# Performance work log

Measured on AMD Instinct MI355X. Metric: run time of the kernel, lower is better.

## Reference

```python
import jax, jax.numpy as jnp
import numpy as np

B, H, S, D = 8, 8, 1024, 64

def setup_inputs() -> dict:
    key = jax.random.key(0)
    kq, kk, kv = jax.random.split(key, 3)
    queries = jax.random.normal(kq, (B, H, S, D), dtype=jnp.float32)
    keys = jax.random.normal(kk, (B, H, S, D), dtype=jnp.float32)
    values = jax.random.normal(kv, (B, H, S, D), dtype=jnp.float32)
    return {"queries": queries, "keys": keys, "values": values}

def reference(queries, keys, values):
    # scale = 1/sqrt(D) since self.scale is None
    scale = 1.0 / jnp.sqrt(jnp.asarray(queries.shape[-1], queries.dtype))
    # scores: [B, H, S, S]
    scores = jnp.einsum("bhqd,bhkd->bhqk", queries, keys) * scale
    # mask_flag=False -> no masking; dropout treated as identity (eval mode)
    attn = jax.nn.softmax(scores, axis=-1)
    output = jnp.einsum("bhqk,bhkd->bhqd", attn, values)
    return (output, attn)
```

## Files before the change

kernel.cpp:

```cpp
#include <hip/hip_runtime.h>
#include <hip/hip_bf16.h>

#define B_ 8
#define H_ 8
#define S_ 1024
#define D_ 64

typedef __attribute__((ext_vector_type(8))) short bf16x8;
typedef __attribute__((ext_vector_type(4))) short bf16x4;
typedef __attribute__((ext_vector_type(4))) float f32x4;

__device__ __forceinline__ short f2bf(float f) {
  union { float f; unsigned u; } x; x.f = f;
  unsigned r = (x.u + 0x7FFFu + ((x.u >> 16) & 1u)) >> 16;
  return (short)r;
}

__global__ __launch_bounds__(256) void cvt_qk(const float* __restrict__ Q,
                                              const float* __restrict__ K,
                                              short* __restrict__ Qb,
                                              short* __restrict__ Kb) {
  const float* in = blockIdx.y ? K : Q;
  short* out      = blockIdx.y ? Kb : Qb;
  const size_t i = ((size_t)blockIdx.x * 256 + threadIdx.x) * 8;
  float4 a = *(const float4*)(in + i);
  float4 b = *(const float4*)(in + i + 4);
  bf16x8 f;
  f[0] = f2bf(a.x); f[1] = f2bf(a.y); f[2] = f2bf(a.z); f[3] = f2bf(a.w);
  f[4] = f2bf(b.x); f[5] = f2bf(b.y); f[6] = f2bf(b.z); f[7] = f2bf(b.w);
  *(bf16x8*)(out + i) = f;
}

__global__ __launch_bounds__(256) void vtrans(const float* __restrict__ V,
                                              short* __restrict__ Vt) {
  const int bh = blockIdx.y;
  const int s0 = blockIdx.x * 64;
  __shared__ float tile[64][65];
  const float* Vb = V + ((size_t)bh * S_ + s0) * D_;
  const int t = threadIdx.x;
  {
    const int rbase = t >> 4;
    const int c4 = (t & 15) * 4;
    #pragma unroll
    for (int i = 0; i < 4; ++i) {
      const int row = i * 16 + rbase;
      float4 v = *(const float4*)(Vb + (size_t)row * D_ + c4);
      tile[row][c4 + 0] = v.x; tile[row][c4 + 1] = v.y;
      tile[row][c4 + 2] = v.z; tile[row][c4 + 3] = v.w;
    }
  }
  __syncthreads();
  const int d = t >> 2;
  const int sq = (t & 3) * 16;
  short* op = Vt + ((size_t)bh * D_ + d) * S_ + s0 + sq;
  bf16x8 a, b;
  #pragma unroll
  for (int j = 0; j < 8; ++j) {
    a[j] = f2bf(tile[sq + j][d]);
    b[j] = f2bf(tile[sq + 8 + j][d]);
  }
  *(bf16x8*)op = a;
  *(bf16x8*)(op + 8) = b;
}

constexpr int QT  = 16;
constexpr int NW  = 4;
constexpr int TPW = (S_ / 16) / NW;

__global__ __launch_bounds__(256, 4) void attn_fused(
    const short* __restrict__ Qb16, const short* __restrict__ Kb16,
    const short* __restrict__ Vt,
    float* __restrict__ O, float* __restrict__ A)
{
  const int nwg = (S_ / QT) * B_ * H_;
  const int cpx = nwg / 8;
  const int lin = blockIdx.x;
  const int swz = (lin & 7) * cpx + (lin >> 3);
  const int bh  = swz / (S_ / QT);
  const int q0  = (swz % (S_ / QT)) * QT;

  const int tid  = threadIdx.x;
  const int wave = tid >> 6;
  const int lane = tid & 63;
  const int m    = lane & 15;
  const int quad = lane >> 4;

  const short* Qb  = Qb16 + (size_t)bh * S_ * D_;
  const short* Kb  = Kb16 + (size_t)bh * S_ * D_;
  const short* Vtb = Vt   + (size_t)bh * D_ * S_;
  float* Ob = O + (size_t)bh * S_ * D_;
  float* Ab = A + (size_t)bh * S_ * S_;

  __shared__ float redmax[NW][QT];
  __shared__ float redsum[NW][QT];
  __shared__ float obuf[NW][QT][D_ + 4];

  bf16x8 qf0, qf1;
  {
    const short* qp = Qb + (size_t)(q0 + m) * D_ + quad * 8;
    qf0 = *(const bf16x8*)qp;
    qf1 = *(const bf16x8*)(qp + 32);
  }

  const short* kbase = Kb + (size_t)m * D_ + quad * 8;
  f32x4 acc[TPW];
  bf16x8 ka0[4], ka1[4];
  #pragma unroll
  for (int p = 0; p < 3; ++p) {
    const short* kp = kbase + (size_t)((p * NW + wave) * 16) * D_;
    ka0[p] = *(const bf16x8*)kp;
    ka1[p] = *(const bf16x8*)(kp + 32);
  }
  #pragma unroll
  for (int t = 0; t < TPW; ++t) {
    if (t + 3 < TPW) {
      const short* kp = kbase + (size_t)(((t + 3) * NW + wave) * 16) * D_;
      ka0[(t + 3) & 3] = *(const bf16x8*)kp;
      ka1[(t + 3) & 3] = *(const bf16x8*)(kp + 32);
    }
    f32x4 c = {0.f, 0.f, 0.f, 0.f};
    c = __builtin_amdgcn_mfma_f32_16x16x32_bf16(ka0[t & 3], qf0, c, 0, 0, 0);
    c = __builtin_amdgcn_mfma_f32_16x16x32_bf16(ka1[t & 3], qf1, c, 0, 0, 0);
    acc[t] = c;
  }

  float mx[TPW];
  #pragma unroll
  for (int t = 0; t < TPW; ++t)
    mx[t] = fmaxf(fmaxf(acc[t][0], acc[t][1]), fmaxf(acc[t][2], acc[t][3]));
  #pragma unroll
  for (int sstep = TPW / 2; sstep > 0; sstep >>= 1) {
    #pragma unroll
    for (int t = 0; t < sstep; ++t) mx[t] = fmaxf(mx[t], mx[t + sstep]);
  }
  float vmax = mx[0];
  vmax = fmaxf(vmax, __shfl_xor(vmax, 16));
  vmax = fmaxf(vmax, __shfl_xor(vmax, 32));

  constexpr float CE = 0.125f * 1.4426950408889634f;
  float sm[TPW];
  #pragma unroll
  for (int t = 0; t < TPW; ++t) {
    float e0 = __builtin_exp2f((acc[t][0] - vmax) * CE);
    float e1 = __builtin_exp2f((acc[t][1] - vmax) * CE);
    float e2 = __builtin_exp2f((acc[t][2] - vmax) * CE);
    float e3 = __builtin_exp2f((acc[t][3] - vmax) * CE);
    acc[t][0] = e0; acc[t][1] = e1; acc[t][2] = e2; acc[t][3] = e3;
    sm[t] = (e0 + e1) + (e2 + e3);
  }
  #pragma unroll
  for (int sstep = TPW / 2; sstep > 0; sstep >>= 1) {
    #pragma unroll
    for (int t = 0; t < sstep; ++t) sm[t] += sm[t + sstep];
  }
  float psum = sm[0];
  psum += __shfl_xor(psum, 16);
  psum += __shfl_xor(psum, 32);

  if (lane < 16) {
    redmax[wave][lane] = vmax;
    redsum[wave][lane] = psum;
  }
  __syncthreads();

  float m0 = redmax[0][m], m1 = redmax[1][m], m2 = redmax[2][m], m3 = redmax[3][m];
  const float gmax = fmaxf(fmaxf(m0, m1), fmaxf(m2, m3));
  float sumg = redsum[0][m] * __builtin_exp2f((m0 - gmax) * CE)
             + redsum[1][m] * __builtin_exp2f((m1 - gmax) * CE)
             + redsum[2][m] * __builtin_exp2f((m2 - gmax) * CE)
             + redsum[3][m] * __builtin_exp2f((m3 - gmax) * CE);
  const float rinv = __builtin_exp2f((vmax - gmax) * CE) / sumg;

  const short* vbase = Vtb + (size_t)m * S_ + quad * 4;
  bf16x4 vb[4][4];
  #pragma unroll
  for (int p = 0; p < 3; ++p) {
    const short* vp = vbase + (p * NW + wave) * 16;
    #pragma unroll
    for (int i = 0; i < 4; ++i)
      vb[p][i] = *(const bf16x4*)(vp + (size_t)(16 * i) * S_);
  }

  f32x4 oc0 = {0.f,0.f,0.f,0.f}, oc1 = {0.f,0.f,0.f,0.f};
  f32x4 oc2 = {0.f,0.f,0.f,0.f}, oc3 = {0.f,0.f,0.f,0.f};
  float* arow = Ab + (size_t)(q0 + m) * S_ + quad * 4;
  #pragma unroll
  for (int t = 0; t < TPW; ++t) {
    if (t + 3 < TPW) {
      const short* vp = vbase + ((t + 3) * NW + wave) * 16;
      #pragma unroll
      for (int i = 0; i < 4; ++i)
        vb[(t + 3) & 3][i] = *(const bf16x4*)(vp + (size_t)(16 * i) * S_);
    }
    const int kt = t * NW + wave;
    f32x4 pn = acc[t] * rinv;
    __builtin_nontemporal_store(pn, (f32x4*)(arow + kt * 16));
    bf16x4 pa;
    pa[0] = f2bf(pn[0]); pa[1] = f2bf(pn[1]);
    pa[2] = f2bf(pn[2]); pa[3] = f2bf(pn[3]);
    oc0 = __builtin_amdgcn_mfma_f32_16x16x16bf16_1k(pa, vb[t & 3][0], oc0, 0, 0, 0);
    oc1 = __builtin_amdgcn_mfma_f32_16x16x16bf16_1k(pa, vb[t & 3][1], oc1, 0, 0, 0);
    oc2 = __builtin_amdgcn_mfma_f32_16x16x16bf16_1k(pa, vb[t & 3][2], oc2, 0, 0, 0);
    oc3 = __builtin_amdgcn_mfma_f32_16x16x16bf16_1k(pa, vb[t & 3][3], oc3, 0, 0, 0);
  }

  #pragma unroll
  for (int r = 0; r < 4; ++r) {
    obuf[wave][quad * 4 + r][m]      = oc0[r];
    obuf[wave][quad * 4 + r][16 + m] = oc1[r];
    obuf[wave][quad * 4 + r][32 + m] = oc2[r];
    obuf[wave][quad * 4 + r][48 + m] = oc3[r];
  }
  __syncthreads();
  {
    const int q  = tid >> 4;
    const int d4 = (tid & 15) * 4;
    f32x4 o0 = *(const f32x4*)&obuf[0][q][d4];
    f32x4 o1 = *(const f32x4*)&obuf[1][q][d4];
    f32x4 o2 = *(const f32x4*)&obuf[2][q][d4];
    f32x4 o3 = *(const f32x4*)&obuf[3][q][d4];
    f32x4 o = (o0 + o1) + (o2 + o3);
    *(f32x4*)&Ob[(size_t)(q0 + q) * D_ + d4] = o;
  }
}

extern "C" void kernel_launch(void* const* d_in, const int* in_sizes, int n_in,
                              void* d_out, int out_size, void* d_ws, size_t ws_size,
                              hipStream_t stream) {
  const float* Q = (const float*)d_in[0];
  const float* K = (const float*)d_in[1];
  const float* V = (const float*)d_in[2];
  float* O = (float*)d_out;
  float* A = O + (size_t)B_ * H_ * S_ * D_;

  const size_t NEL = (size_t)B_ * H_ * S_ * D_;
  short* Qbf = (short*)d_ws;
  short* Kbf = Qbf + NEL;
  short* Vtb = Kbf + NEL;

  const int cvt_blocks = (int)(NEL / 8 / 256);
  cvt_qk<<<dim3(cvt_blocks, 2), 256, 0, stream>>>(Q, K, Qbf, Kbf);
  vtrans<<<dim3(S_ / 64, B_ * H_), 256, 0, stream>>>(V, Vtb);

  attn_fused<<<(S_ / QT) * B_ * H_, NW * 64, 0, stream>>>(Qbf, Kbf, Vtb, O, A);
}
```

Baseline: 471.5 us.

## Stage attention-probability rows through LDS for coalesced full-row stores

Remaps each wave's key tiles to contiguous 64-column blocks within 256-column groups. Each group of normalized probabilities is staged into a double-buffered LDS chunk, then written to global memory as coalesced 1 KB row segments. The old path issued scattered 16-byte nontemporal stores per lane. The change also drops the register prefetch ring for V fragments and loads them inline, and adds a block barrier per group, which may expose more load latency.

Result: faster. 459.3 us (-2.6%).

```diff
diff --git a/kernel.cpp b/kernel.cpp
--- a/kernel.cpp
+++ b/kernel.cpp
@@ -66,6 +66,7 @@
 constexpr int QT  = 16;
 constexpr int NW  = 4;
 constexpr int TPW = (S_ / 16) / NW;
+constexpr int CH_STRIDE = 260;
 
 __global__ __launch_bounds__(256, 4) void attn_fused(
     const short* __restrict__ Qb16, const short* __restrict__ Kb16,
@@ -91,9 +92,9 @@
   float* Ob = O + (size_t)bh * S_ * D_;
   float* Ab = A + (size_t)bh * S_ * S_;
 
+  __shared__ float smem[2 * 16 * CH_STRIDE];
   __shared__ float redmax[NW][QT];
   __shared__ float redsum[NW][QT];
-  __shared__ float obuf[NW][QT][D_ + 4];
 
   bf16x8 qf0, qf1;
   {
@@ -107,16 +108,19 @@
   bf16x8 ka0[4], ka1[4];
   #pragma unroll
   for (int p = 0; p < 3; ++p) {
-    const short* kp = kbase + (size_t)((p * NW + wave) * 16) * D_;
+    const int row = wave * 64 + p * 16;
+    const short* kp = kbase + (size_t)row * D_;
     ka0[p] = *(const bf16x8*)kp;
     ka1[p] = *(const bf16x8*)(kp + 32);
   }
   #pragma unroll
   for (int t = 0; t < TPW; ++t) {
     if (t + 3 < TPW) {
-      const short* kp = kbase + (size_t)(((t + 3) * NW + wave) * 16) * D_;
-      ka0[(t + 3) & 3] = *(const bf16x8*)kp;
-      ka1[(t + 3) & 3] = *(const bf16x8*)(kp + 32);
+      const int tn = t + 3;
+      const int row = (tn >> 2) * 256 + wave * 64 + (tn & 3) * 16;
+      const short* kp = kbase + (size_t)row * D_;
+      ka0[tn & 3] = *(const bf16x8*)kp;
+      ka1[tn & 3] = *(const bf16x8*)(kp + 32);
     }
     f32x4 c = {0.f, 0.f, 0.f, 0.f};
     c = __builtin_amdgcn_mfma_f32_16x16x32_bf16(ka0[t & 3], qf0, c, 0, 0, 0);
@@ -172,53 +176,58 @@
   const float rinv = __builtin_exp2f((vmax - gmax) * CE) / sumg;
 
   const short* vbase = Vtb + (size_t)m * S_ + quad * 4;
-  bf16x4 vb[4][4];
-  #pragma unroll
-  for (int p = 0; p < 3; ++p) {
-    const short* vp = vbase + (p * NW + wave) * 16;
-    #pragma unroll
-    for (int i = 0; i < 4; ++i)
-      vb[p][i] = *(const bf16x4*)(vp + (size_t)(16 * i) * S_);
-  }
-
   f32x4 oc0 = {0.f,0.f,0.f,0.f}, oc1 = {0.f,0.f,0.f,0.f};
   f32x4 oc2 = {0.f,0.f,0.f,0.f}, oc3 = {0.f,0.f,0.f,0.f};
-  float* arow = Ab + (size_t)(q0 + m) * S_ + quad * 4;
-  #pragma unroll
-  for (int t = 0; t < TPW; ++t) {
-    if (t + 3 < TPW) {
-      const short* vp = vbase + ((t + 3) * NW + wave) * 16;
-      #pragma unroll
-      for (int i = 0; i < 4; ++i)
-        vb[(t + 3) & 3][i] = *(const bf16x4*)(vp + (size_t)(16 * i) * S_);
-    }
-    const int kt = t * NW + wave;
-    f32x4 pn = acc[t] * rinv;
-    __builtin_nontemporal_store(pn, (f32x4*)(arow + kt * 16));
-    bf16x4 pa;
-    pa[0] = f2bf(pn[0]); pa[1] = f2bf(pn[1]);
-    pa[2] = f2bf(pn[2]); pa[3] = f2bf(pn[3]);
-    oc0 = __builtin_amdgcn_mfma_f32_16x16x16bf16_1k(pa, vb[t & 3][0], oc0, 0, 0, 0);
-    oc1 = __builtin_amdgcn_mfma_f32_16x16x16bf16_1k(pa, vb[t & 3][1], oc1, 0, 0, 0);
-    oc2 = __builtin_amdgcn_mfma_f32_16x16x16bf16_1k(pa, vb[t & 3][2], oc2, 0, 0, 0);
-    oc3 = __builtin_amdgcn_mfma_f32_16x16x16bf16_1k(pa, vb[t & 3][3], oc3, 0, 0, 0);
-  }
-
-  #pragma unroll
-  for (int r = 0; r < 4; ++r) {
-    obuf[wave][quad * 4 + r][m]      = oc0[r];
-    obuf[wave][quad * 4 + r][16 + m] = oc1[r];
-    obuf[wave][quad * 4 + r][32 + m] = oc2[r];
-    obuf[wave][quad * 4 + r][48 + m] = oc3[r];
+
+  #pragma unroll
+  for (int g = 0; g < 4; ++g) {
+    float* chunk = smem + (g & 1) * (16 * CH_STRIDE);
+    #pragma unroll
+    for (int c = 0; c < 4; ++c) {
+      const int t = g * 4 + c;
+      const int kcol = g * 256 + wave * 64 + c * 16;
+      f32x4 pn = acc[t] * rinv;
+      *(f32x4*)&chunk[m * CH_STRIDE + wave * 64 + c * 16 + quad * 4] = pn;
+      bf16x4 pa;
+      pa[0] = f2bf(pn[0]); pa[1] = f2bf(pn[1]);
+      pa[2] = f2bf(pn[2]); pa[3] = f2bf(pn[3]);
+      const short* vp = vbase + kcol;
+      bf16x4 bv0 = *(const bf16x4*)(vp);
+      bf16x4 bv1 = *(const bf16x4*)(vp + (size_t)16 * S_);
+      bf16x4 bv2 = *(const bf16x4*)(vp + (size_t)32 * S_);
+      bf16x4 bv3 = *(const bf16x4*)(vp + (size_t)48 * S_);
+      oc0 = __builtin_amdgcn_mfma_f32_16x16x16bf16_1k(pa, bv0, oc0, 0, 0, 0);
+      oc1 = __builtin_amdgcn_mfma_f32_16x16x16bf16_1k(pa, bv1, oc1, 0, 0, 0);
+      oc2 = __builtin_amdgcn_mfma_f32_16x16x16bf16_1k(pa, bv2, oc2, 0, 0, 0);
+      oc3 = __builtin_amdgcn_mfma_f32_16x16x16bf16_1k(pa, bv3, oc3, 0, 0, 0);
+    }
+    __syncthreads();
+    #pragma unroll
+    for (int rep = 0; rep < 4; ++rep) {
+      const int row = rep * 4 + wave;
+      const f32x4 v = *(const f32x4*)&chunk[row * CH_STRIDE + lane * 4];
+      *(f32x4*)&Ab[(size_t)(q0 + row) * S_ + g * 256 + lane * 4] = v;
+    }
   }
   __syncthreads();
+
   {
+    float* obuf = smem;
+    #pragma unroll
+    for (int r = 0; r < 4; ++r) {
+      float* orow = obuf + (wave * QT + quad * 4 + r) * 68;
+      orow[m]      = oc0[r];
+      orow[16 + m] = oc1[r];
+      orow[32 + m] = oc2[r];
+      orow[48 + m] = oc3[r];
+    }
+    __syncthreads();
     const int q  = tid >> 4;
     const int d4 = (tid & 15) * 4;
-    f32x4 o0 = *(const f32x4*)&obuf[0][q][d4];
-    f32x4 o1 = *(const f32x4*)&obuf[1][q][d4];
-    f32x4 o2 = *(const f32x4*)&obuf[2][q][d4];
-    f32x4 o3 = *(const f32x4*)&obuf[3][q][d4];
+    f32x4 o0 = *(const f32x4*)&obuf[(0 * QT + q) * 68 + d4];
+    f32x4 o1 = *(const f32x4*)&obuf[(1 * QT + q) * 68 + d4];
+    f32x4 o2 = *(const f32x4*)&obuf[(2 * QT + q) * 68 + d4];
+    f32x4 o3 = *(const f32x4*)&obuf[(3 * QT + q) * 68 + d4];
     f32x4 o = (o0 + o1) + (o2 + o3);
     *(f32x4*)&Ob[(size_t)(q0 + q) * D_ + d4] = o;
   }
```
